# Optimization experiments

Measured on AMD Instinct MI355X. Metric: run time of the kernel, lower is better.

Reference implementation:

```python
import jax, jax.numpy as jnp
import numpy as np

HEADS = 4
DIM_HEAD = 32
SCALE = DIM_HEAD ** -0.5


def setup_inputs() -> dict:
    key = jax.random.key(0)
    k1, k2, k3 = jax.random.split(key, 3)
    B, C, H, W = 4, 128, 64, 64
    inner = HEADS * DIM_HEAD  # 128
    x = jax.random.normal(k1, (B, C, H, W), dtype=jnp.float32)
    # 1x1 conv weights == channel-mixing matrices [out_ch, in_ch]
    w_qkv = jax.random.normal(k2, (inner * 3, C), dtype=jnp.float32) * (C ** -0.5)
    w_proj = jax.random.normal(k3, (C, inner), dtype=jnp.float32) * (inner ** -0.5)
    b_proj = jnp.zeros((C,), dtype=jnp.float32)
    return {"x": x, "w_qkv": w_qkv, "w_proj": w_proj, "b_proj": b_proj}


def reference(x, w_qkv, w_proj, b_proj):
    b, c, h, w = x.shape
    n = h * w
    # 1x1 conv = per-pixel matmul over channels
    qkv = jnp.einsum('bchw,oc->bohw', x, w_qkv)  # [B, 3*inner, H, W]
    q, k, v = jnp.split(qkv, 3, axis=1)

    def to_heads(t):
        # [B, inner, H, W] -> [B, heads, HW, dim_head]
        return t.reshape(b, HEADS, DIM_HEAD, n).transpose(0, 1, 3, 2)

    q = to_heads(q) * SCALE
    k = to_heads(k)
    v = to_heads(v)
    # scores [B, heads, HW, HW]; softmax is max-stabilized (matches torch amax-subtract)
    scores = jnp.einsum('bhnd,bhmd->bhnm', q, k)
    attn = jax.nn.softmax(scores, axis=-1)
    out = jnp.einsum('bhnm,bhmd->bhnd', attn, v)  # [B, heads, HW, dim_head]
    out = out.transpose(0, 1, 3, 2).reshape(b, HEADS * DIM_HEAD, h, w)
    return jnp.einsum('bchw,oc->bohw', out, w_proj) + b_proj[None, :, None, None]
```

## Files before the change

### kernel.cpp

```cpp
#include <hip/hip_runtime.h>

typedef _Float16 f16;
typedef unsigned short u16;
typedef __attribute__((ext_vector_type(8))) f16 f16x8;
typedef __attribute__((ext_vector_type(4))) f16 f16x4;
typedef __attribute__((ext_vector_type(4))) float floatx4;

#define NPIX 4096
#define KT   128
#define VROW 136

__global__ __launch_bounds__(256) void qkv_mfma(
    const float* __restrict__ x, const float* __restrict__ w,
    f16* __restrict__ qh, f16* __restrict__ kh, f16* __restrict__ vth)
{
    __shared__ f16 wlds[64 * 136];
    const int tid  = threadIdx.x;
    const int wave = tid >> 6;
    const int lane = tid & 63;
    const int quad = lane >> 4;
    const int l16  = lane & 15;
    const int pbase = blockIdx.x * 64;
    const int y     = blockIdx.y;
    const int b     = blockIdx.z;

#pragma unroll
    for (int i = 0; i < 8; ++i) {
        int idx = i * 256 + tid;
        int o = idx >> 5, ch = idx & 31;
        float4 wv = *(const float4*)(w + (size_t)(y * 64 + o) * 128 + ch * 4);
        f16x4 h; h[0] = (f16)wv.x; h[1] = (f16)wv.y; h[2] = (f16)wv.z; h[3] = (f16)wv.w;
        *(f16x4*)&wlds[o * 136 + ch * 4] = h;
    }
    __syncthreads();

    const float* xb = x + (size_t)b * 128 * NPIX;
    const int type = y >> 1;

    if (type < 2) {
        const int p_row = pbase + wave * 16 + l16;
        f16x8 af[4];
#pragma unroll
        for (int kc = 0; kc < 4; ++kc) {
            const int c0 = kc * 32 + quad * 8;
#pragma unroll
            for (int j = 0; j < 8; ++j)
                af[kc][j] = (f16)xb[(size_t)(c0 + j) * NPIX + p_row];
        }
        floatx4 acc[4];
#pragma unroll
        for (int n = 0; n < 4; ++n) acc[n] = floatx4{0.f, 0.f, 0.f, 0.f};
#pragma unroll
        for (int n = 0; n < 4; ++n)
#pragma unroll
            for (int kc = 0; kc < 4; ++kc) {
                f16x8 bf = *(const f16x8*)&wlds[(n * 16 + l16) * 136 + kc * 32 + quad * 8];
                acc[n] = __builtin_amdgcn_mfma_f32_16x16x32_f16(af[kc], bf, acc[n], 0, 0, 0);
            }
        const float qs = (type == 0) ? 0.17677669529663687f * 1.4426950408889634f : 1.0f;
        f16* dst = (type == 0) ? qh : kh;
#pragma unroll
        for (int n = 0; n < 4; ++n) {
            const int og   = y * 64 + n * 16 + l16;
            const int head = (og >> 5) & 3;
            const int d    = og & 31;
            f16* base = dst + (size_t)(b * 4 + head) * NPIX * 32;
#pragma unroll
            for (int r = 0; r < 4; ++r) {
                const int p = pbase + wave * 16 + quad * 4 + r;
                base[(size_t)p * 32 + d] = (f16)(acc[n][r] * qs);
            }
        }
    } else {
        const int p_col = pbase + wave * 16 + l16;
        f16x8 bf[4];
#pragma unroll
        for (int kc = 0; kc < 4; ++kc) {
            const int c0 = kc * 32 + quad * 8;
#pragma unroll
            for (int j = 0; j < 8; ++j)
                bf[kc][j] = (f16)xb[(size_t)(c0 + j) * NPIX + p_col];
        }
        floatx4 acc[4];
#pragma unroll
        for (int m = 0; m < 4; ++m) acc[m] = floatx4{0.f, 0.f, 0.f, 0.f};
#pragma unroll
        for (int m = 0; m < 4; ++m)
#pragma unroll
            for (int kc = 0; kc < 4; ++kc) {
                f16x8 af = *(const f16x8*)&wlds[(m * 16 + l16) * 136 + kc * 32 + quad * 8];
                acc[m] = __builtin_amdgcn_mfma_f32_16x16x32_f16(af, bf[kc], acc[m], 0, 0, 0);
            }
#pragma unroll
        for (int m = 0; m < 4; ++m)
#pragma unroll
            for (int r = 0; r < 4; ++r) {
                const int og   = y * 64 + m * 16 + quad * 4 + r;
                const int head = (og >> 5) & 3;
                const int d    = og & 31;
                vth[((size_t)(b * 4 + head) * 32 + d) * NPIX + p_col] = (f16)acc[m][r];
            }
    }
}

__global__ __launch_bounds__(256, 2) void attn_kernel(
    const f16* __restrict__ qh, const f16* __restrict__ kh,
    const f16* __restrict__ vth, f16* __restrict__ att)
{
    __shared__ f16 klds[KT * 32];
    __shared__ f16 vlds[32 * VROW];

    const int tid  = threadIdx.x;
    const int wave = tid >> 6;
    const int lane = tid & 63;
    const int quad = lane >> 4;
    const int l16  = lane & 15;
    const int bh   = blockIdx.y;
    const int qbase = blockIdx.x * 128 + wave * 32;

    const f16* kb = kh + (size_t)bh * NPIX * 32;
    const f16* vb = vth + (size_t)bh * 32 * NPIX;

    f16x8 qB[2];
#pragma unroll
    for (int h = 0; h < 2; ++h)
        qB[h] = *(const f16x8*)(qh + ((size_t)bh * NPIX + qbase + h * 16 + l16) * 32 + quad * 8);

    floatx4 oacc[2][2];
#pragma unroll
    for (int h = 0; h < 2; ++h)
#pragma unroll
        for (int dh = 0; dh < 2; ++dh) oacc[h][dh] = floatx4{0.f, 0.f, 0.f, 0.f};
    float lsum[2] = {0.f, 0.f};

    for (int kt = 0; kt < NPIX / KT; ++kt) {
        __syncthreads();
        {
            const int4* src = (const int4*)(kb + (size_t)kt * KT * 32);
            ((int4*)klds)[tid]       = src[tid];
            ((int4*)klds)[tid + 256] = src[tid + 256];
        }
        {
            const int r  = tid >> 3;
            const int cc = (tid & 7) * 2;
            const int4* vsrc = (const int4*)(vb + (size_t)r * NPIX + kt * KT + cc * 8);
            int4 v0 = vsrc[0], v1 = vsrc[1];
            int4* vdst = (int4*)(vlds + r * VROW + cc * 8);
            vdst[0] = v0; vdst[1] = v1;
        }
        __syncthreads();

        f16x8 kf[8];
#pragma unroll
        for (int t = 0; t < 8; ++t)
            kf[t] = *(const f16x8*)&klds[(t * 16 + l16) * 32 + quad * 8];
        f16x4 vf[8][2];
#pragma unroll
        for (int c = 0; c < 8; ++c)
#pragma unroll
            for (int dh = 0; dh < 2; ++dh)
                vf[c][dh] = *(const f16x4*)&vlds[(dh * 16 + l16) * VROW + c * 16 + quad * 4];

#pragma unroll
        for (int h = 0; h < 2; ++h) {
            floatx4 st[8];
#pragma unroll
            for (int t = 0; t < 8; ++t) {
                floatx4 z = {0.f, 0.f, 0.f, 0.f};
                st[t] = __builtin_amdgcn_mfma_f32_16x16x32_f16(kf[t], qB[h], z, 0, 0, 0);
            }
            f16x4 pf[8];
            float ls = 0.f;
#pragma unroll
            for (int c = 0; c < 8; ++c)
#pragma unroll
                for (int r = 0; r < 4; ++r) {
                    float e = __builtin_amdgcn_exp2f(st[c][r]);
                    ls += e;
                    pf[c][r] = (f16)e;
                }
            lsum[h] += ls;
#pragma unroll
            for (int c = 0; c < 8; ++c) {
                oacc[h][0] = __builtin_amdgcn_mfma_f32_16x16x16f16(pf[c], vf[c][0], oacc[h][0], 0, 0, 0);
                oacc[h][1] = __builtin_amdgcn_mfma_f32_16x16x16f16(pf[c], vf[c][1], oacc[h][1], 0, 0, 0);
            }
        }
    }

#pragma unroll
    for (int h = 0; h < 2; ++h) {
        float l = lsum[h];
        l += __shfl_xor(l, 16);
        l += __shfl_xor(l, 32);
        const float inv = 1.0f / l;
#pragma unroll
        for (int r = 0; r < 4; ++r) {
            const float invr = __shfl(inv, quad * 4 + r);
            const int q = qbase + h * 16 + quad * 4 + r;
            f16* ob = att + ((size_t)bh * NPIX + q) * 32;
            ob[l16]      = (f16)(oacc[h][0][r] * invr);
            ob[16 + l16] = (f16)(oacc[h][1][r] * invr);
        }
    }
}

__global__ __launch_bounds__(256) void proj_mfma(
    const f16* __restrict__ att, const float* __restrict__ wp,
    const float* __restrict__ bp, float* __restrict__ out)
{
    __shared__ f16 wplds[128 * 136];
    __shared__ float bplds[128];
    const int tid  = threadIdx.x;
    const int wave = tid >> 6;
    const int lane = tid & 63;
    const int quad = lane >> 4;
    const int l16  = lane & 15;
    const int pbase = blockIdx.x * 64;
    const int b     = blockIdx.y;

    if (tid < 128) bplds[tid] = bp[tid];
#pragma unroll
    for (int i = 0; i < 16; ++i) {
        int idx = i * 256 + tid;
        int o = idx >> 5, ch = idx & 31;
        float4 wv = *(const float4*)(wp + (size_t)o * 128 + ch * 4);
        f16x4 h; h[0] = (f16)wv.x; h[1] = (f16)wv.y; h[2] = (f16)wv.z; h[3] = (f16)wv.w;
        *(f16x4*)&wplds[o * 136 + ch * 4] = h;
    }
    __syncthreads();

    const f16* ab = att + (size_t)b * 4 * NPIX * 32;
    const int p_col = pbase + wave * 16 + l16;
    f16x8 bf[4];
#pragma unroll
    for (int kc = 0; kc < 4; ++kc)
        bf[kc] = *(const f16x8*)(ab + ((size_t)kc * NPIX + p_col) * 32 + quad * 8);

    floatx4 acc[8];
#pragma unroll
    for (int m = 0; m < 8; ++m) acc[m] = floatx4{0.f, 0.f, 0.f, 0.f};
#pragma unroll
    for (int m = 0; m < 8; ++m)
#pragma unroll
        for (int kc = 0; kc < 4; ++kc) {
            f16x8 af = *(const f16x8*)&wplds[(m * 16 + l16) * 136 + kc * 32 + quad * 8];
            acc[m] = __builtin_amdgcn_mfma_f32_16x16x32_f16(af, bf[kc], acc[m], 0, 0, 0);
        }

#pragma unroll
    for (int m = 0; m < 8; ++m)
#pragma unroll
        for (int r = 0; r < 4; ++r) {
            const int o = m * 16 + quad * 4 + r;
            out[((size_t)b * 128 + o) * NPIX + p_col] = acc[m][r] + bplds[o];
        }
}

extern "C" void kernel_launch(void* const* d_in, const int* in_sizes, int n_in,
                              void* d_out, int out_size, void* d_ws, size_t ws_size,
                              hipStream_t stream)
{
    const float* x      = (const float*)d_in[0];
    const float* w_qkv  = (const float*)d_in[1];
    const float* w_proj = (const float*)d_in[2];
    const float* b_proj = (const float*)d_in[3];
    float* out = (float*)d_out;

    char* ws = (char*)d_ws;
    f16* qh  = (f16*)(ws);
    f16* kh  = (f16*)(ws + (4u << 20));
    f16* vth = (f16*)(ws + (8u << 20));
    f16* att = (f16*)(ws + (12u << 20));

    qkv_mfma<<<dim3(64, 6, 4), 256, 0, stream>>>(x, w_qkv, qh, kh, vth);
    attn_kernel<<<dim3(32, 16, 1), 256, 0, stream>>>(qh, kh, vth, att);
    proj_mfma<<<dim3(64, 4, 1), 256, 0, stream>>>(att, w_proj, b_proj, out);
}
```

Before: 128.6 us.

## Pre-convert weights, fuse QKV outputs per block, and shrink attention tiles

Adds a small kernel that converts the QKV and projection weights to fp16 once, folding the softmax scale into Q, so the GEMM kernels read fp16 weights straight from global memory with no LDS staging. The QKV kernel now loads each x tile once and loops over all six output groups instead of launching one block per group. The attention kernel processes 16 queries per wave instead of 32, launches 1024 blocks with a remapped (batch-head, query-block) order, raises launch bounds to 4 blocks per CU, and uses 16x16x32 MFMAs with packed conversions for the PV product. In exchange, each attention block reloads the same K/V tiles for half as many queries, doubling K/V traffic, and there is one extra kernel launch.

```diff
diff --git a/kernel.cpp b/kernel.cpp
--- a/kernel.cpp
+++ b/kernel.cpp
@@ -1,109 +1,112 @@
 #include <hip/hip_runtime.h>
 
 typedef _Float16 f16;
-typedef unsigned short u16;
 typedef __attribute__((ext_vector_type(8))) f16 f16x8;
 typedef __attribute__((ext_vector_type(4))) f16 f16x4;
+typedef __attribute__((ext_vector_type(2))) __fp16 h16x2;
 typedef __attribute__((ext_vector_type(4))) float floatx4;
 
 #define NPIX 4096
 #define KT   128
 #define VROW 136
 
+__global__ __launch_bounds__(256) void cvt_w(
+    const float* __restrict__ wq, const float* __restrict__ wp,
+    f16* __restrict__ wh, f16* __restrict__ wph)
+{
+    const int idx = (blockIdx.x * 256 + threadIdx.x) * 4;
+    const float qs = 0.17677669529663687f * 1.4426950408889634f;
+    float4 v;
+    f16* dst;
+    if (idx < 49152) { v = *(const float4*)(wq + idx); dst = wh + idx; }
+    else             { v = *(const float4*)(wp + (idx - 49152)); dst = wph + (idx - 49152); }
+    if (idx < 16384) { v.x *= qs; v.y *= qs; v.z *= qs; v.w *= qs; }
+    h16x2 a = __builtin_amdgcn_cvt_pkrtz(v.x, v.y);
+    h16x2 b = __builtin_amdgcn_cvt_pkrtz(v.z, v.w);
+    f16x4 h; h[0] = (f16)a[0]; h[1] = (f16)a[1]; h[2] = (f16)b[0]; h[3] = (f16)b[1];
+    *(f16x4*)dst = h;
+}
+
 __global__ __launch_bounds__(256) void qkv_mfma(
-    const float* __restrict__ x, const float* __restrict__ w,
+    const float* __restrict__ x, const f16* __restrict__ wh,
     f16* __restrict__ qh, f16* __restrict__ kh, f16* __restrict__ vth)
 {
-    __shared__ f16 wlds[64 * 136];
     const int tid  = threadIdx.x;
     const int wave = tid >> 6;
     const int lane = tid & 63;
     const int quad = lane >> 4;
     const int l16  = lane & 15;
     const int pbase = blockIdx.x * 64;
-    const int y     = blockIdx.y;
-    const int b     = blockIdx.z;
-
-#pragma unroll
-    for (int i = 0; i < 8; ++i) {
-        int idx = i * 256 + tid;
-        int o = idx >> 5, ch = idx & 31;
-        float4 wv = *(const float4*)(w + (size_t)(y * 64 + o) * 128 + ch * 4);
-        f16x4 h; h[0] = (f16)wv.x; h[1] = (f16)wv.y; h[2] = (f16)wv.z; h[3] = (f16)wv.w;
-        *(f16x4*)&wlds[o * 136 + ch * 4] = h;
-    }
-    __syncthreads();
+    const int b     = blockIdx.y;
+    const int p_col = pbase + wave * 16 + l16;
 
     const float* xb = x + (size_t)b * 128 * NPIX;
-    const int type = y >> 1;
-
-    if (type < 2) {
-        const int p_row = pbase + wave * 16 + l16;
-        f16x8 af[4];
-#pragma unroll
-        for (int kc = 0; kc < 4; ++kc) {
-            const int c0 = kc * 32 + quad * 8;
-#pragma unroll
-            for (int j = 0; j < 8; ++j)
-                af[kc][j] = (f16)xb[(size_t)(c0 + j) * NPIX + p_row];
-        }
+
+    f16x8 xf[4];
+#pragma unroll
+    for (int kc = 0; kc < 4; ++kc) {
+        const int c0 = kc * 32 + quad * 8;
+        float e[8];
+#pragma unroll
+        for (int j = 0; j < 8; ++j)
+            e[j] = xb[(size_t)(c0 + j) * NPIX + p_col];
+#pragma unroll
+        for (int j = 0; j < 4; ++j) {
+            h16x2 pk = __builtin_amdgcn_cvt_pkrtz(e[2 * j], e[2 * j + 1]);
+            xf[kc][2 * j] = (f16)pk[0]; xf[kc][2 * j + 1] = (f16)pk[1];
+        }
+    }
+
+#pragma unroll
+    for (int y = 0; y < 6; ++y) {
         floatx4 acc[4];
 #pragma unroll
-        for (int n = 0; n < 4; ++n) acc[n] = floatx4{0.f, 0.f, 0.f, 0.f};
-#pragma unroll
-        for (int n = 0; n < 4; ++n)
-#pragma unroll
-            for (int kc = 0; kc < 4; ++kc) {
-                f16x8 bf = *(const f16x8*)&wlds[(n * 16 + l16) * 136 + kc * 32 + quad * 8];
-                acc[n] = __builtin_amdgcn_mfma_f32_16x16x32_f16(af[kc], bf, acc[n], 0, 0, 0);
+        for (int i = 0; i < 4; ++i) acc[i] = floatx4{0.f, 0.f, 0.f, 0.f};
+
+        if (y < 4) {
+#pragma unroll
+            for (int n = 0; n < 4; ++n)
+#pragma unroll
+                for (int kc = 0; kc < 4; ++kc) {
+                    f16x8 wf = *(const f16x8*)&wh[(size_t)(y * 64 + n * 16 + l16) * 128 + kc * 32 + quad * 8];
+                    acc[n] = __builtin_amdgcn_mfma_f32_16x16x32_f16(xf[kc], wf, acc[n], 0, 0, 0);
+                }
+            f16* dst = (y < 2) ? qh : kh;
+#pragma unroll
+            for (int n = 0; n < 4; ++n) {
+                const int og    = y * 64 + n * 16 + l16;
+                const int local = og & 127;
+                const int head  = local >> 5;
+                const int d     = local & 31;
+                f16* base = dst + (size_t)(b * 4 + head) * NPIX * 32;
+#pragma unroll
+                for (int r = 0; r < 4; ++r) {
+                    const int p = pbase + wave * 16 + quad * 4 + r;
+                    base[(size_t)p * 32 + d] = (f16)acc[n][r];
+                }
             }
-        const float qs = (type == 0) ? 0.17677669529663687f * 1.4426950408889634f : 1.0f;
-        f16* dst = (type == 0) ? qh : kh;
-#pragma unroll
-        for (int n = 0; n < 4; ++n) {
-            const int og   = y * 64 + n * 16 + l16;
-            const int head = (og >> 5) & 3;
-            const int d    = og & 31;
-            f16* base = dst + (size_t)(b * 4 + head) * NPIX * 32;
-#pragma unroll
-            for (int r = 0; r < 4; ++r) {
-                const int p = pbase + wave * 16 + quad * 4 + r;
-                base[(size_t)p * 32 + d] = (f16)(acc[n][r] * qs);
-            }
-        }
-    } else {
-        const int p_col = pbase + wave * 16 + l16;
-        f16x8 bf[4];
-#pragma unroll
-        for (int kc = 0; kc < 4; ++kc) {
-            const int c0 = kc * 32 + quad * 8;
-#pragma unroll
-            for (int j = 0; j < 8; ++j)
-                bf[kc][j] = (f16)xb[(size_t)(c0 + j) * NPIX + p_col];
-        }
-        floatx4 acc[4];
-#pragma unroll
-        for (int m = 0; m < 4; ++m) acc[m] = floatx4{0.f, 0.f, 0.f, 0.f};
-#pragma unroll
-        for (int m = 0; m < 4; ++m)
-#pragma unroll
-            for (int kc = 0; kc < 4; ++kc) {
-                f16x8 af = *(const f16x8*)&wlds[(m * 16 + l16) * 136 + kc * 32 + quad * 8];
-                acc[m] = __builtin_amdgcn_mfma_f32_16x16x32_f16(af, bf[kc], acc[m], 0, 0, 0);
-            }
-#pragma unroll
-        for (int m = 0; m < 4; ++m)
-#pragma unroll
-            for (int r = 0; r < 4; ++r) {
-                const int og   = y * 64 + m * 16 + quad * 4 + r;
-                const int head = (og >> 5) & 3;
-                const int d    = og & 31;
-                vth[((size_t)(b * 4 + head) * 32 + d) * NPIX + p_col] = (f16)acc[m][r];
-            }
-    }
-}
-
-__global__ __launch_bounds__(256, 2) void attn_kernel(
+        } else {
+#pragma unroll
+            for (int m = 0; m < 4; ++m)
+#pragma unroll
+                for (int kc = 0; kc < 4; ++kc) {
+                    f16x8 wf = *(const f16x8*)&wh[(size_t)(y * 64 + m * 16 + l16) * 128 + kc * 32 + quad * 8];
+                    acc[m] = __builtin_amdgcn_mfma_f32_16x16x32_f16(wf, xf[kc], acc[m], 0, 0, 0);
+                }
+#pragma unroll
+            for (int m = 0; m < 4; ++m)
+#pragma unroll
+                for (int r = 0; r < 4; ++r) {
+                    const int ov   = (y - 4) * 64 + m * 16 + quad * 4 + r;
+                    const int head = ov >> 5;
+                    const int d    = ov & 31;
+                    vth[((size_t)(b * 4 + head) * 32 + d) * NPIX + p_col] = (f16)acc[m][r];
+                }
+        }
+    }
+}
+
+__global__ __launch_bounds__(256, 4) void attn_kernel(
     const f16* __restrict__ qh, const f16* __restrict__ kh,
     const f16* __restrict__ vth, f16* __restrict__ att)
 {
@@ -115,23 +118,21 @@
     const int lane = tid & 63;
     const int quad = lane >> 4;
     const int l16  = lane & 15;
-    const int bh   = blockIdx.y;
-    const int qbase = blockIdx.x * 128 + wave * 32;
+
+    const int n    = blockIdx.x;
+    const int bh   = (n & 7) * 2 + ((n >> 3) & 1);
+    const int qblk = n >> 4;
+    const int qbase = qblk * 64 + wave * 16;
 
     const f16* kb = kh + (size_t)bh * NPIX * 32;
     const f16* vb = vth + (size_t)bh * 32 * NPIX;
 
-    f16x8 qB[2];
-#pragma unroll
-    for (int h = 0; h < 2; ++h)
-        qB[h] = *(const f16x8*)(qh + ((size_t)bh * NPIX + qbase + h * 16 + l16) * 32 + quad * 8);
-
-    floatx4 oacc[2][2];
-#pragma unroll
-    for (int h = 0; h < 2; ++h)
-#pragma unroll
-        for (int dh = 0; dh < 2; ++dh) oacc[h][dh] = floatx4{0.f, 0.f, 0.f, 0.f};
-    float lsum[2] = {0.f, 0.f};
+    f16x8 qB = *(const f16x8*)(qh + ((size_t)bh * NPIX + qbase + l16) * 32 + quad * 8);
+
+    floatx4 oacc[2];
+    oacc[0] = floatx4{0.f, 0.f, 0.f, 0.f};
+    oacc[1] = floatx4{0.f, 0.f, 0.f, 0.f};
+    float lsum = 0.f;
 
     for (int kt = 0; kt < NPIX / KT; ++kt) {
         __syncthreads();
@@ -150,67 +151,64 @@
         }
         __syncthreads();
 
-        f16x8 kf[8];
-#pragma unroll
-        for (int t = 0; t < 8; ++t)
-            kf[t] = *(const f16x8*)&klds[(t * 16 + l16) * 32 + quad * 8];
-        f16x4 vf[8][2];
-#pragma unroll
-        for (int c = 0; c < 8; ++c)
-#pragma unroll
-            for (int dh = 0; dh < 2; ++dh)
-                vf[c][dh] = *(const f16x4*)&vlds[(dh * 16 + l16) * VROW + c * 16 + quad * 4];
-
-#pragma unroll
-        for (int h = 0; h < 2; ++h) {
-            floatx4 st[8];
-#pragma unroll
-            for (int t = 0; t < 8; ++t) {
-                floatx4 z = {0.f, 0.f, 0.f, 0.f};
-                st[t] = __builtin_amdgcn_mfma_f32_16x16x32_f16(kf[t], qB[h], z, 0, 0, 0);
+        floatx4 st[8];
+#pragma unroll
+        for (int t = 0; t < 8; ++t) {
+            f16x8 kf = *(const f16x8*)&klds[(t * 16 + l16) * 32 + quad * 8];
+            floatx4 z = {0.f, 0.f, 0.f, 0.f};
+            st[t] = __builtin_amdgcn_mfma_f32_16x16x32_f16(kf, qB, z, 0, 0, 0);
+        }
+
+        f16x4 paf[8];
+#pragma unroll
+        for (int t = 0; t < 8; ++t) {
+            float e0 = __builtin_amdgcn_exp2f(st[t][0]);
+            float e1 = __builtin_amdgcn_exp2f(st[t][1]);
+            float e2 = __builtin_amdgcn_exp2f(st[t][2]);
+            float e3 = __builtin_amdgcn_exp2f(st[t][3]);
+            lsum += (e0 + e1) + (e2 + e3);
+            h16x2 lo = __builtin_amdgcn_cvt_pkrtz(e0, e1);
+            h16x2 hi = __builtin_amdgcn_cvt_pkrtz(e2, e3);
+            paf[t][0] = (f16)lo[0]; paf[t][1] = (f16)lo[1];
+            paf[t][2] = (f16)hi[0]; paf[t][3] = (f16)hi[1];
+        }
+
+#pragma unroll
+        for (int g = 0; g < 4; ++g) {
+            f16x8 pA;
+#pragma unroll
+            for (int j = 0; j < 4; ++j) { pA[j] = paf[2 * g][j]; pA[4 + j] = paf[2 * g + 1][j]; }
+#pragma unroll
+            for (int dh = 0; dh < 2; ++dh) {
+                const f16* vrow = &vlds[(dh * 16 + l16) * VROW + 32 * g + quad * 4];
+                f16x4 v0 = *(const f16x4*)(vrow);
+                f16x4 v1 = *(const f16x4*)(vrow + 16);
+                f16x8 vB;
+#pragma unroll
+                for (int j = 0; j < 4; ++j) { vB[j] = v0[j]; vB[4 + j] = v1[j]; }
+                oacc[dh] = __builtin_amdgcn_mfma_f32_16x16x32_f16(pA, vB, oacc[dh], 0, 0, 0);
             }
-            f16x4 pf[8];
-            float ls = 0.f;
-#pragma unroll
-            for (int c = 0; c < 8; ++c)
-#pragma unroll
-                for (int r = 0; r < 4; ++r) {
-                    float e = __builtin_amdgcn_exp2f(st[c][r]);
-                    ls += e;
-                    pf[c][r] = (f16)e;
-                }
-            lsum[h] += ls;
-#pragma unroll
-            for (int c = 0; c < 8; ++c) {
-                oacc[h][0] = __builtin_amdgcn_mfma_f32_16x16x16f16(pf[c], vf[c][0], oacc[h][0], 0, 0, 0);
-                oacc[h][1] = __builtin_amdgcn_mfma_f32_16x16x16f16(pf[c], vf[c][1], oacc[h][1], 0, 0, 0);
-            }
-        }
-    }
-
-#pragma unroll
-    for (int h = 0; h < 2; ++h) {
-        float l = lsum[h];
-        l += __shfl_xor(l, 16);
-        l += __shfl_xor(l, 32);
-        const float inv = 1.0f / l;
-#pragma unroll
-        for (int r = 0; r < 4; ++r) {
-            const float invr = __shfl(inv, quad * 4 + r);
-            const int q = qbase + h * 16 + quad * 4 + r;
-            f16* ob = att + ((size_t)bh * NPIX + q) * 32;
-            ob[l16]      = (f16)(oacc[h][0][r] * invr);
-            ob[16 + l16] = (f16)(oacc[h][1][r] * invr);
-        }
+        }
+    }
+
+    float l = lsum;
+    l += __shfl_xor(l, 16);
+    l += __shfl_xor(l, 32);
+    const float inv = 1.0f / l;
+#pragma unroll
+    for (int r = 0; r < 4; ++r) {
+        const float invr = __shfl(inv, quad * 4 + r);
+        const int q = qbase + quad * 4 + r;
+        f16* ob = att + ((size_t)bh * NPIX + q) * 32;
+        ob[l16]      = (f16)(oacc[0][r] * invr);
+        ob[16 + l16] = (f16)(oacc[1][r] * invr);
     }
 }
 
 __global__ __launch_bounds__(256) void proj_mfma(
-    const f16* __restrict__ att, const float* __restrict__ wp,
+    const f16* __restrict__ att, const f16* __restrict__ wph,
     const float* __restrict__ bp, float* __restrict__ out)
 {
-    __shared__ f16 wplds[128 * 136];
-    __shared__ float bplds[128];
     const int tid  = threadIdx.x;
     const int wave = tid >> 6;
     const int lane = tid & 63;
@@ -218,20 +216,9 @@
     const int l16  = lane & 15;
     const int pbase = blockIdx.x * 64;
     const int b     = blockIdx.y;
-
-    if (tid < 128) bplds[tid] = bp[tid];
-#pragma unroll
-    for (int i = 0; i < 16; ++i) {
-        int idx = i * 256 + tid;
-        int o = idx >> 5, ch = idx & 31;
-        float4 wv = *(const float4*)(wp + (size_t)o * 128 + ch * 4);
-        f16x4 h; h[0] = (f16)wv.x; h[1] = (f16)wv.y; h[2] = (f16)wv.z; h[3] = (f16)wv.w;
-        *(f16x4*)&wplds[o * 136 + ch * 4] = h;
-    }
-    __syncthreads();
+    const int p_col = pbase + wave * 16 + l16;
 
     const f16* ab = att + (size_t)b * 4 * NPIX * 32;
-    const int p_col = pbase + wave * 16 + l16;
     f16x8 bf[4];
 #pragma unroll
     for (int kc = 0; kc < 4; ++kc)
@@ -244,7 +231,7 @@
     for (int m = 0; m < 8; ++m)
 #pragma unroll
         for (int kc = 0; kc < 4; ++kc) {
-            f16x8 af = *(const f16x8*)&wplds[(m * 16 + l16) * 136 + kc * 32 + quad * 8];
+            f16x8 af = *(const f16x8*)&wph[(size_t)(m * 16 + l16) * 128 + kc * 32 + quad * 8];
             acc[m] = __builtin_amdgcn_mfma_f32_16x16x32_f16(af, bf[kc], acc[m], 0, 0, 0);
         }
 
@@ -253,7 +240,7 @@
 #pragma unroll
         for (int r = 0; r < 4; ++r) {
             const int o = m * 16 + quad * 4 + r;
-            out[((size_t)b * 128 + o) * NPIX + p_col] = acc[m][r] + bplds[o];
+            out[((size_t)b * 128 + o) * NPIX + p_col] = acc[m][r] + bp[o];
         }
 }
 
@@ -272,8 +259,11 @@
     f16* kh  = (f16*)(ws + (4u << 20));
     f16* vth = (f16*)(ws + (8u << 20));
     f16* att = (f16*)(ws + (12u << 20));
-
-    qkv_mfma<<<dim3(64, 6, 4), 256, 0, stream>>>(x, w_qkv, qh, kh, vth);
-    attn_kernel<<<dim3(32, 16, 1), 256, 0, stream>>>(qh, kh, vth, att);
-    proj_mfma<<<dim3(64, 4, 1), 256, 0, stream>>>(att, w_proj, b_proj, out);
-}
+    f16* wh  = (f16*)(ws + (16u << 20));
+    f16* wph = (f16*)(ws + (16u << 20) + (96u << 10));
+
+    cvt_w<<<dim3(64, 1, 1), 256, 0, stream>>>(w_qkv, w_proj, wh, wph);
+    qkv_mfma<<<dim3(64, 4, 1), 256, 0, stream>>>(x, wh, qh, kh, vth);
+    attn_kernel<<<dim3(1024, 1, 1), 256, 0, stream>>>(qh, kh, vth, att);
+    proj_mfma<<<dim3(64, 4, 1), 256, 0, stream>>>(att, wph, b_proj, out);
+}
```

Result: slower. 153.0 us (+19.0%).
